# Performance work log

Measured on AMD Instinct MI355X. Metric: run time of the kernel, lower is better.

The kernel has to match this reference:

```python
import jax, jax.numpy as jnp
import numpy as np

NUM_EMBEDDINGS = 1024
EMBEDDING_DIM = 256
COMMITMENT_COST = 0.25


def setup_inputs() -> dict:
    key = jax.random.key(0)
    k1, k2 = jax.random.split(key)
    z = jax.random.normal(k1, (64, 32, 32, EMBEDDING_DIM), dtype=jnp.float32)
    # torch init: uniform(-1/num_embeddings, 1/num_embeddings)
    codebook = jax.random.uniform(
        k2, (NUM_EMBEDDINGS, EMBEDDING_DIM), dtype=jnp.float32,
        minval=-1.0 / NUM_EMBEDDINGS, maxval=1.0 / NUM_EMBEDDINGS)
    return {"z": z, "codebook": codebook}


def reference(z, codebook):
    sg = jax.lax.stop_gradient
    D = codebook.shape[1]
    flat_z = z.reshape(-1, D)  # [N, D]
    # squared L2 distances: ||z||^2 + ||e||^2 - 2 z.e  -> [N, K]
    distances = (jnp.sum(flat_z * flat_z, axis=1, keepdims=True)
                 + jnp.sum(codebook * codebook, axis=1)
                 - 2.0 * jnp.matmul(flat_z, codebook.T))
    indices = jnp.argmin(distances, axis=1)  # [N]
    quantized = codebook[indices].reshape(z.shape)
    e_latent_loss = jnp.mean((quantized - sg(z)) ** 2)
    q_latent_loss = jnp.mean((z - sg(quantized)) ** 2)
    vq_loss = e_latent_loss + COMMITMENT_COST * q_latent_loss
    # straight-through estimator
    quantized_st = z + sg(quantized - z)
    return quantized_st, vq_loss, indices.reshape(z.shape[:-1])
```

## Files before the change

kernel.cpp:

```cpp
#include <hip/hip_runtime.h>

#pragma clang fp contract(off)


#define NROWS   65536
#define DDIM    256
#define KCODES  1024
#define QSIZE   (NROWS * DDIM)
#define LOSS_OFF QSIZE
#define IDX_OFF (QSIZE + 1)
#define MARGIN  3.0e-4f
#define RCAP    16384
#define RBATCH  16

typedef __bf16 bf16x8 __attribute__((ext_vector_type(8)));
typedef float f32x4 __attribute__((ext_vector_type(4)));
typedef unsigned int u32;
typedef unsigned long long u64;
typedef unsigned short u16;

#define GLOAD_LDS16(gsrc, ldst) \
    __builtin_amdgcn_global_load_lds( \
        (const __attribute__((address_space(1))) u32*)(gsrc), \
        (__attribute__((address_space(3))) u32*)(ldst), 16, 0, 0)

__device__ __forceinline__ u32 omap(float s) {
    u32 u = __float_as_uint(s);
    return (u & 0x80000000u) ? ~u : (u | 0x80000000u);
}
__device__ __forceinline__ u64 pack_key(float s, u32 j) {
    return ((u64)omap(s) << 32) | j;
}

__device__ __forceinline__ float pw128_sq(const float* __restrict__ x) {
    float r[8];
    #pragma unroll
    for (int j = 0; j < 8; ++j) r[j] = x[j] * x[j];
    for (int i = 8; i < 128; i += 8)
        #pragma unroll
        for (int j = 0; j < 8; ++j) r[j] += x[i + j] * x[i + j];
    return ((r[0] + r[1]) + (r[2] + r[3])) + ((r[4] + r[5]) + (r[6] + r[7]));
}

__global__ __launch_bounds__(256) void vq_pack_cb(
    const float* __restrict__ E, u16* __restrict__ ebh,
    float* __restrict__ ee, float* __restrict__ sum, int* __restrict__ count) {
    int j = blockIdx.x * 256 + threadIdx.x;
    if (j == 0) { *sum = 0.0f; *count = 0; }
    if (j >= KCODES) return;
    const float* row = E + (size_t)j * DDIM;
    #pragma unroll
    for (int ks = 0; ks < 32; ++ks) {
        bf16x8 h8;
        #pragma unroll
        for (int e = 0; e < 8; ++e) h8[e] = (__bf16)row[ks * 8 + e];
        *(bf16x8*)(ebh + ((size_t)ks * KCODES + j) * 8) = h8;
    }
    ee[j] = pw128_sq(row) + pw128_sq(row + 128);
}

__device__ __forceinline__ void stage_chunk(
    const u16* __restrict__ ebh, int chbase, char* buf, int t) {
    #pragma unroll
    for (int i = 0; i < 8; ++i) {
        int p = t + 256 * i;
        int ks = p >> 6, c = p & 63;
        GLOAD_LDS16(ebh + ((size_t)ks * KCODES + chbase + c) * 8, buf + p * 16);
    }
}

__global__ __launch_bounds__(256, 2) void vq_gemm(
    const float* __restrict__ Z,
    const u16* __restrict__ ebh,
    const float* __restrict__ ee,
    float* out, float* __restrict__ sum, int* __restrict__ count,
    int* __restrict__ list) {
    __shared__ __align__(16) char bs[2][32768];
    const int t = threadIdx.x, w = t >> 6, l = t & 63;
    const int lr = l & 15, lg = l >> 4;
    const int rowbase = blockIdx.x * 128;

    bf16x8 aH[2][8];
    float ss = 0.0f;
    #pragma unroll
    for (int rf = 0; rf < 2; ++rf) {
        const float* zr = Z + (size_t)(rowbase + w * 32 + rf * 16 + lr) * DDIM;
        #pragma unroll
        for (int s = 0; s < 8; ++s) {
            const float4* src = (const float4*)(zr + (s * 4 + lg) * 8);
            float4 v0 = src[0], v1 = src[1];
            bf16x8 h8;
            h8[0] = (__bf16)v0.x; h8[1] = (__bf16)v0.y;
            h8[2] = (__bf16)v0.z; h8[3] = (__bf16)v0.w;
            h8[4] = (__bf16)v1.x; h8[5] = (__bf16)v1.y;
            h8[6] = (__bf16)v1.z; h8[7] = (__bf16)v1.w;
            aH[rf][s] = h8;
            ss += v0.x * v0.x + v0.y * v0.y + v0.z * v0.z + v0.w * v0.w
                + v1.x * v1.x + v1.y * v1.y + v1.z * v1.z + v1.w * v1.w;
        }
    }
    #pragma unroll
    for (int off = 1; off < 64; off <<= 1) ss += __shfl_xor(ss, off);
    if (l == 0) atomicAdd(sum, ss);

    float s1[2][4], s2[2][4]; int i1[2][4];
    #pragma unroll
    for (int rf = 0; rf < 2; ++rf)
        #pragma unroll
        for (int r = 0; r < 4; ++r) { s1[rf][r] = 1e30f; s2[rf][r] = 1e30f; i1[rf][r] = 0x7FFFFFFF; }

    int cur = 0;
    stage_chunk(ebh, 0, bs[0], t);
    for (int ch = 0; ch < 16; ++ch) {
        __syncthreads();
        if (ch + 1 < 16) stage_chunk(ebh, (ch + 1) * 64, bs[cur ^ 1], t);
        const char* buf = bs[cur];
        const int chbase = ch * 64;

        f32x4 acc[2][4];
        #pragma unroll
        for (int rf = 0; rf < 2; ++rf)
            #pragma unroll
            for (int cf = 0; cf < 4; ++cf) acc[rf][cf] = 0.0f;

        #pragma unroll
        for (int s = 0; s < 8; ++s) {
            #pragma unroll
            for (int cf = 0; cf < 4; ++cf) {
                int off = (((s * 4 + lg) * 64 + cf * 16 + lr) * 16);
                bf16x8 bh = *(const bf16x8*)(buf + off);
                #pragma unroll
                for (int rf = 0; rf < 2; ++rf)
                    acc[rf][cf] = __builtin_amdgcn_mfma_f32_16x16x32_bf16(aH[rf][s], bh, acc[rf][cf], 0, 0, 0);
            }
        }
        #pragma unroll
        for (int cf = 0; cf < 4; ++cf) {
            int code = chbase + cf * 16 + lr;
            float e2c = ee[code];
            #pragma unroll
            for (int rf = 0; rf < 2; ++rf)
                #pragma unroll
                for (int r = 0; r < 4; ++r) {
                    float v = __fmaf_rn(-2.0f, acc[rf][cf][r], e2c);
                    float so = s1[rf][r];
                    s2[rf][r] = fminf(fmaxf(so, v), s2[rf][r]);
                    bool lt = v < so;
                    s1[rf][r] = lt ? v : so;
                    i1[rf][r] = lt ? code : i1[rf][r];
                }
        }
        cur ^= 1;
    }
    #pragma unroll
    for (int off = 1; off < 16; off <<= 1) {
        #pragma unroll
        for (int rf = 0; rf < 2; ++rf)
            #pragma unroll
            for (int r = 0; r < 4; ++r) {
                float os1 = __shfl_xor(s1[rf][r], off);
                float os2 = __shfl_xor(s2[rf][r], off);
                int   oi  = __shfl_xor(i1[rf][r], off);
                float ns2 = fminf(fmaxf(s1[rf][r], os1), fminf(s2[rf][r], os2));
                bool take = (os1 < s1[rf][r]) || (os1 == s1[rf][r] && oi < i1[rf][r]);
                s1[rf][r] = take ? os1 : s1[rf][r];
                i1[rf][r] = take ? oi : i1[rf][r];
                s2[rf][r] = ns2;
            }
    }
    if (lr == 0) {
        float lsum = 0.0f;
        #pragma unroll
        for (int rf = 0; rf < 2; ++rf)
            #pragma unroll
            for (int r = 0; r < 4; ++r) {
                int row = rowbase + w * 32 + rf * 16 + lg * 4 + r;
                out[(size_t)IDX_OFF + row] = (float)i1[rf][r];
                lsum += s1[rf][r];
                if (s2[rf][r] <= s1[rf][r] + MARGIN) {
                    int slot = atomicAdd(count, 1);
                    if (slot < RCAP) list[slot] = row;
                }
            }
        atomicAdd(sum, lsum);
    }
}

__global__ __launch_bounds__(256) void vq_rescue(
    const float* __restrict__ Z, const float* __restrict__ E,
    const float* __restrict__ ee, const int* __restrict__ count,
    const int* __restrict__ list, float* out) {
    __shared__ float zrow[RBATCH][DDIM];
    __shared__ float zacc[RBATCH][16];
    __shared__ float z2s[RBATCH];
    __shared__ u64 rmin[RBATCH];
    __shared__ int rowid[RBATCH];
    int n = *count; if (n > RCAP) n = RCAP;
    const int t = threadIdx.x;
    const int base = blockIdx.x * RBATCH;
    if (base >= n) return;
    int nb = n - base; if (nb > RBATCH) nb = RBATCH;

    if (t < RBATCH) {
        rowid[t] = (t < nb) ? list[base + t] : 0;
        rmin[t] = ~0ULL;
    }
    __syncthreads();
    #pragma unroll
    for (int i = 0; i < RBATCH * (DDIM / 4) / 256; ++i) {
        int p = t + 256 * i;
        int r = p >> 6, c4 = p & 63;
        if (r < nb) ((float4*)zrow[r])[c4] =
            ((const float4*)(Z + (size_t)rowid[r] * DDIM))[c4];
    }
    __syncthreads();
    if (t < RBATCH * 8) {
        int r = t >> 3, j = t & 7;
        const float* zr = zrow[r];
        float a0 = zr[j] * zr[j], a1 = zr[128 + j] * zr[128 + j];
        for (int i = 8; i < 128; i += 8) {
            a0 += zr[i + j] * zr[i + j];
            a1 += zr[128 + i + j] * zr[128 + i + j];
        }
        zacc[r][j] = a0; zacc[r][8 + j] = a1;
    }
    __syncthreads();
    if (t < RBATCH) {
        const float* a = zacc[t];
        float c0 = ((a[0] + a[1]) + (a[2] + a[3])) + ((a[4] + a[5]) + (a[6] + a[7]));
        float c1 = ((a[8] + a[9]) + (a[10] + a[11])) + ((a[12] + a[13]) + (a[14] + a[15]));
        z2s[t] = c0 + c1;
    }
    __syncthreads();

    float acc[4][RBATCH];
    #pragma unroll
    for (int c = 0; c < 4; ++c)
        #pragma unroll
        for (int r = 0; r < RBATCH; ++r) acc[c][r] = 0.0f;

    for (int d4 = 0; d4 < DDIM / 4; ++d4) {
        float4 ev[4];
        #pragma unroll
        for (int c = 0; c < 4; ++c)
            ev[c] = ((const float4*)(E + (size_t)(t + c * 256) * DDIM))[d4];
        #pragma unroll
        for (int r = 0; r < RBATCH; ++r) {
            float4 zv = ((const float4*)zrow[r])[d4];
            #pragma unroll
            for (int c = 0; c < 4; ++c) {
                float a = acc[c][r];
                a = __fmaf_rn(zv.x, ev[c].x, a); a = __fmaf_rn(zv.y, ev[c].y, a);
                a = __fmaf_rn(zv.z, ev[c].z, a); a = __fmaf_rn(zv.w, ev[c].w, a);
                acc[c][r] = a;
            }
        }
    }
    float e2c[4];
    #pragma unroll
    for (int c = 0; c < 4; ++c) e2c[c] = ee[t + c * 256];
    #pragma unroll
    for (int r = 0; r < RBATCH; ++r) {
        float zr2 = z2s[r];
        u64 best = ~0ULL;
        #pragma unroll
        for (int c = 0; c < 4; ++c) {
            float d = (zr2 + e2c[c]) - 2.0f * acc[c][r];
            u64 k = pack_key(d, (u32)(t + c * 256));
            if (k < best) best = k;
        }
        #pragma unroll
        for (int off = 1; off < 64; off <<= 1) {
            u64 o = __shfl_xor(best, off);
            if (o < best) best = o;
        }
        if ((t & 63) == 0) atomicMin(&rmin[r], best);
    }
    __syncthreads();
    if (t < nb) out[(size_t)IDX_OFF + rowid[t]] = (float)(u32)(rmin[t] & 0xFFFFFFFFu);
}

__global__ __launch_bounds__(256) void vq_qwrite(
    const float* __restrict__ E, const float* __restrict__ sum, float* out) {
    __shared__ int qidx[32];
    const int t = threadIdx.x;
    const size_t rowbase = (size_t)blockIdx.x * 32;
    if (blockIdx.x == 0 && t == 0) out[LOSS_OFF] = 1.25f * (*sum) / (float)QSIZE;
    if (t < 32) qidx[t] = (int)out[(size_t)IDX_OFF + rowbase + t];
    __syncthreads();
    float4* outq = (float4*)out;
    #pragma unroll
    for (int k = 0; k < 8; ++k) {
        int idx = t + 256 * k;
        int r = idx >> 6, c4 = idx & 63;
        int code = qidx[r];
        outq[rowbase * 64 + idx] = ((const float4*)(E + (size_t)code * DDIM))[c4];
    }
}

extern "C" void kernel_launch(void* const* d_in, const int* in_sizes, int n_in,
                              void* d_out, int out_size, void* d_ws, size_t ws_size,
                              hipStream_t stream) {
    const float* Z; const float* E;
    if (in_sizes[0] == QSIZE) { Z = (const float*)d_in[0]; E = (const float*)d_in[1]; }
    else                      { Z = (const float*)d_in[1]; E = (const float*)d_in[0]; }
    float* out = (float*)d_out;
    char* ws = (char*)d_ws;

    float* sum   = (float*)ws;
    int*   count = (int*)(ws + 4);
    float* ee    = (float*)(ws + 1024);
    u16*   ebh   = (u16*)(ws + 8192);
    int*   list  = (int*)(ws + 8192 + 524288);

    vq_pack_cb<<<4, 256, 0, stream>>>(E, ebh, ee, sum, count);
    vq_gemm<<<NROWS / 128, 256, 0, stream>>>(Z, ebh, ee, out, sum, count, list);
    vq_rescue<<<RCAP / RBATCH, 256, 0, stream>>>(Z, E, ee, count, list, out);
    vq_qwrite<<<NROWS / 32, 256, 0, stream>>>(E, sum, out);
}
```

Before: 231.6 us.

## Split codebook search across two blocks per row tile and merge in combine kernel

```diff
diff --git a/kernel.cpp b/kernel.cpp
--- a/kernel.cpp
+++ b/kernel.cpp
@@ -59,26 +59,28 @@
     ee[j] = pw128_sq(row) + pw128_sq(row + 128);
 }
 
-__device__ __forceinline__ void stage_chunk(
-    const u16* __restrict__ ebh, int chbase, char* buf, int t) {
-    #pragma unroll
-    for (int i = 0; i < 8; ++i) {
+__device__ __forceinline__ void stage_chunk32(
+    const u16* __restrict__ ebh, int codebase, char* buf, int t) {
+    #pragma unroll
+    for (int i = 0; i < 4; ++i) {
         int p = t + 256 * i;
-        int ks = p >> 6, c = p & 63;
-        GLOAD_LDS16(ebh + ((size_t)ks * KCODES + chbase + c) * 8, buf + p * 16);
-    }
-}
-
-__global__ __launch_bounds__(256, 2) void vq_gemm(
+        int ks = p >> 5, c = p & 31;
+        GLOAD_LDS16(ebh + ((size_t)ks * KCODES + codebase + c) * 8, buf + p * 16);
+    }
+}
+
+__global__ __launch_bounds__(256, 4) void vq_gemm(
     const float* __restrict__ Z,
     const u16* __restrict__ ebh,
     const float* __restrict__ ee,
-    float* out, float* __restrict__ sum, int* __restrict__ count,
-    int* __restrict__ list) {
-    __shared__ __align__(16) char bs[2][32768];
+    float* __restrict__ s1c, float* __restrict__ s2c, float* __restrict__ i1c,
+    float* __restrict__ sum) {
+    __shared__ __align__(16) char bs[2][16384];
     const int t = threadIdx.x, w = t >> 6, l = t & 63;
     const int lr = l & 15, lg = l >> 4;
-    const int rowbase = blockIdx.x * 128;
+    const int rowtile = blockIdx.x >> 1, half = blockIdx.x & 1;
+    const int rowbase = rowtile * 128;
+    const int codebase = half * 512;
 
     bf16x8 aH[2][8];
     float ss = 0.0f;
@@ -99,9 +101,11 @@
                 + v1.x * v1.x + v1.y * v1.y + v1.z * v1.z + v1.w * v1.w;
         }
     }
-    #pragma unroll
-    for (int off = 1; off < 64; off <<= 1) ss += __shfl_xor(ss, off);
-    if (l == 0) atomicAdd(sum, ss);
+    if (half == 0) {
+        #pragma unroll
+        for (int off = 1; off < 64; off <<= 1) ss += __shfl_xor(ss, off);
+        if (l == 0) atomicAdd(sum, ss);
+    }
 
     float s1[2][4], s2[2][4]; int i1[2][4];
     #pragma unroll
@@ -110,24 +114,24 @@
         for (int r = 0; r < 4; ++r) { s1[rf][r] = 1e30f; s2[rf][r] = 1e30f; i1[rf][r] = 0x7FFFFFFF; }
 
     int cur = 0;
-    stage_chunk(ebh, 0, bs[0], t);
+    stage_chunk32(ebh, codebase, bs[0], t);
     for (int ch = 0; ch < 16; ++ch) {
         __syncthreads();
-        if (ch + 1 < 16) stage_chunk(ebh, (ch + 1) * 64, bs[cur ^ 1], t);
+        if (ch + 1 < 16) stage_chunk32(ebh, codebase + (ch + 1) * 32, bs[cur ^ 1], t);
         const char* buf = bs[cur];
-        const int chbase = ch * 64;
-
-        f32x4 acc[2][4];
+        const int chbase = codebase + ch * 32;
+
+        f32x4 acc[2][2];
         #pragma unroll
         for (int rf = 0; rf < 2; ++rf)
             #pragma unroll
-            for (int cf = 0; cf < 4; ++cf) acc[rf][cf] = 0.0f;
+            for (int cf = 0; cf < 2; ++cf) acc[rf][cf] = 0.0f;
 
         #pragma unroll
         for (int s = 0; s < 8; ++s) {
             #pragma unroll
-            for (int cf = 0; cf < 4; ++cf) {
-                int off = (((s * 4 + lg) * 64 + cf * 16 + lr) * 16);
+            for (int cf = 0; cf < 2; ++cf) {
+                int off = (((s * 4 + lg) * 32 + cf * 16 + lr) * 16);
                 bf16x8 bh = *(const bf16x8*)(buf + off);
                 #pragma unroll
                 for (int rf = 0; rf < 2; ++rf)
@@ -135,7 +139,7 @@
             }
         }
         #pragma unroll
-        for (int cf = 0; cf < 4; ++cf) {
+        for (int cf = 0; cf < 2; ++cf) {
             int code = chbase + cf * 16 + lr;
             float e2c = ee[code];
             #pragma unroll
@@ -169,34 +173,53 @@
             }
     }
     if (lr == 0) {
-        float lsum = 0.0f;
         #pragma unroll
         for (int rf = 0; rf < 2; ++rf)
             #pragma unroll
             for (int r = 0; r < 4; ++r) {
-                int row = rowbase + w * 32 + rf * 16 + lg * 4 + r;
-                out[(size_t)IDX_OFF + row] = (float)i1[rf][r];
-                lsum += s1[rf][r];
-                if (s2[rf][r] <= s1[rf][r] + MARGIN) {
-                    int slot = atomicAdd(count, 1);
-                    if (slot < RCAP) list[slot] = row;
-                }
+                size_t idx = (size_t)half * NROWS + rowbase + w * 32 + rf * 16 + lg * 4 + r;
+                s1c[idx] = s1[rf][r];
+                s2c[idx] = s2[rf][r];
+                i1c[idx] = (float)i1[rf][r];
             }
-        atomicAdd(sum, lsum);
-    }
+    }
+}
+
+__global__ __launch_bounds__(256) void vq_combine(
+    const float* __restrict__ s1c, const float* __restrict__ s2c,
+    const float* __restrict__ i1c,
+    float* out, float* __restrict__ sum, int* __restrict__ count,
+    int* __restrict__ list) {
+    const int r = blockIdx.x * 256 + threadIdx.x;
+    float s1a = s1c[r], s1b = s1c[NROWS + r];
+    float s2a = s2c[r], s2b = s2c[NROWS + r];
+    int   ia  = (int)i1c[r], ib = (int)i1c[NROWS + r];
+    bool tb = s1b < s1a;
+    float s1 = tb ? s1b : s1a;
+    int   i1 = tb ? ib : ia;
+    float s2 = tb ? fminf(s2b, s1a) : fminf(s2a, s1b);
+    out[(size_t)IDX_OFF + r] = (float)i1;
+    if (s2 <= s1 + MARGIN) {
+        int slot = atomicAdd(count, 1);
+        if (slot < RCAP) list[slot] = r;
+    }
+    #pragma unroll
+    for (int off = 1; off < 64; off <<= 1) s1 += __shfl_xor(s1, off);
+    if ((threadIdx.x & 63) == 0) atomicAdd(sum, s1);
 }
 
 __global__ __launch_bounds__(256) void vq_rescue(
     const float* __restrict__ Z, const float* __restrict__ E,
     const float* __restrict__ ee, const int* __restrict__ count,
-    const int* __restrict__ list, float* out) {
+    const int* __restrict__ list, const float* __restrict__ sum, float* out) {
     __shared__ float zrow[RBATCH][DDIM];
     __shared__ float zacc[RBATCH][16];
     __shared__ float z2s[RBATCH];
     __shared__ u64 rmin[RBATCH];
     __shared__ int rowid[RBATCH];
+    const int t = threadIdx.x;
+    if (blockIdx.x == 0 && t == 0) out[LOSS_OFF] = 1.25f * (*sum) / (float)QSIZE;
     int n = *count; if (n > RCAP) n = RCAP;
-    const int t = threadIdx.x;
     const int base = blockIdx.x * RBATCH;
     if (base >= n) return;
     int nb = n - base; if (nb > RBATCH) nb = RBATCH;
@@ -281,11 +304,10 @@
 }
 
 __global__ __launch_bounds__(256) void vq_qwrite(
-    const float* __restrict__ E, const float* __restrict__ sum, float* out) {
+    const float* __restrict__ E, float* out) {
     __shared__ int qidx[32];
     const int t = threadIdx.x;
     const size_t rowbase = (size_t)blockIdx.x * 32;
-    if (blockIdx.x == 0 && t == 0) out[LOSS_OFF] = 1.25f * (*sum) / (float)QSIZE;
     if (t < 32) qidx[t] = (int)out[(size_t)IDX_OFF + rowbase + t];
     __syncthreads();
     float4* outq = (float4*)out;
@@ -313,8 +335,13 @@
     u16*   ebh   = (u16*)(ws + 8192);
     int*   list  = (int*)(ws + 8192 + 524288);
 
+    float* s1c = out;
+    float* s2c = out + 2 * NROWS;
+    float* i1c = out + 4 * NROWS;
+
     vq_pack_cb<<<4, 256, 0, stream>>>(E, ebh, ee, sum, count);
-    vq_gemm<<<NROWS / 128, 256, 0, stream>>>(Z, ebh, ee, out, sum, count, list);
-    vq_rescue<<<RCAP / RBATCH, 256, 0, stream>>>(Z, E, ee, count, list, out);
-    vq_qwrite<<<NROWS / 32, 256, 0, stream>>>(E, sum, out);
-}
+    vq_gemm<<<NROWS / 128 * 2, 256, 0, stream>>>(Z, ebh, ee, s1c, s2c, i1c, sum);
+    vq_combine<<<NROWS / 256, 256, 0, stream>>>(s1c, s2c, i1c, out, sum, count, list);
+    vq_rescue<<<RCAP / RBATCH, 256, 0, stream>>>(Z, E, ee, count, list, sum, out);
+    vq_qwrite<<<NROWS / 32, 256, 0, stream>>>(E, out);
+}
```

Result: slower. 249.1 us (+7.5%).
